# Optimization experiments

Measured on AMD Instinct MI355X. Metric: run time of the kernel, lower is better.

The kernel has to match this reference:

```python
import jax, jax.numpy as jnp
import numpy as np
from functools import partial

C_IN = 32
KT = 10  # 3*3 taps + bias


def avgpool(x, k):
    B, C, H, W = x.shape
    return x.reshape(B, C, H // k, k, W // k, k).mean(axis=(3, 5))


def conv3x3(x, w, b):
    out = jax.lax.conv_general_dilated(
        x, w, window_strides=(1, 1), padding=[(1, 1), (1, 1)],
        dimension_numbers=("NCHW", "OIHW", "NCHW"))
    return out + b[None, :, None, None]


def conv1x1(x, w, b):
    # w: [O, C, 1, 1]
    return jnp.einsum("bchw,oc->bohw", x, w[:, :, 0, 0]) + b[None, :, None, None]


def predictor(x, w1, b1, w2, b2):
    return x + conv3x3(jax.nn.leaky_relu(conv3x3(x, w1, b1), 0.01), w2, b2)


def flying_conv(x, weight, bias):
    # x: [B,C,H,W]; weight: [B,C,Hb,Wb,9]; bias: [B,C,Hb,Wb]; 8x8 blocks
    B, C, H, W = x.shape
    Hb, Wb = H // 8, W // 8
    xp = jnp.pad(x, ((0, 0), (0, 0), (1, 1), (1, 1)))
    out = jnp.broadcast_to(bias[:, :, :, None, :, None], (B, C, Hb, 8, Wb, 8))
    for k in range(9):
        di, dj = k // 3, k % 3
        xs = xp[:, :, di:di + H, dj:dj + W].reshape(B, C, Hb, 8, Wb, 8)
        out = out + xs * weight[:, :, :, None, :, None, k]
    return out.reshape(B, C, H, W)


def setup_inputs() -> dict:
    key = jax.random.key(0)
    ks = jax.random.split(key, 5)
    B, C, H, W = 4, C_IN, 512, 512
    x = jax.random.normal(ks[0], (B, C, H, W), dtype=jnp.float32)
    pa_w = jax.random.normal(ks[1], (4, 2, C, C, 3, 3), dtype=jnp.float32) * 0.05
    pa_b = jnp.zeros((4, 2, C), dtype=jnp.float32)
    exp_w = jax.random.normal(ks[2], (C * KT, C, 1, 1), dtype=jnp.float32) * 0.05
    exp_b = jnp.zeros((C * KT,), dtype=jnp.float32)
    pw_w = jax.random.normal(ks[3], (C, C, 1, 1), dtype=jnp.float32) * 0.1
    pw_b = jnp.zeros((C,), dtype=jnp.float32)
    return {"x": x, "pa_w": pa_w, "pa_b": pa_b, "exp_w": exp_w,
            "exp_b": exp_b, "pw_w": pw_w, "pw_b": pw_b}


def reference(x, pa_w, pa_b, exp_w, exp_b, pw_w, pw_b):
    B, C, H, W = x.shape
    feat = avgpool(x, 4)  # H/4
    for i in range(4):
        feat = predictor(feat, pa_w[i, 0], pa_b[i, 0], pa_w[i, 1], pa_b[i, 1])
        if i == 1:
            feat = avgpool(feat, 2)  # -> H/8
    wmap = conv1x1(feat, exp_w, exp_b)  # [B, C*10, Hb, Wb]
    Hb, Wb = H // 8, W // 8
    wmap = jnp.tanh(wmap.reshape(B, C, KT, Hb, Wb).transpose(0, 1, 3, 4, 2))
    weight, bias = wmap[..., :9], wmap[..., 9]
    out = flying_conv(x, weight, bias)
    return conv1x1(out, pw_w, pw_b)
```

## Files before the change

kernel.cpp:

```cpp
#include <hip/hip_runtime.h>


#define BATCH 4
#define NCH 32
#define CS128 17680
#define SP128 136
#define CS64 4752
#define SP64 72

__device__ __forceinline__ float fast_tanh(float s) {
  float e = __expf(2.f * s);
  return fmaf(-2.f, __builtin_amdgcn_rcpf(e + 1.f), 1.f);
}

__global__ void zero_kernel(float* __restrict__ p) {
  int i = blockIdx.x * 256 + threadIdx.x;
  *reinterpret_cast<float4*>(p + (size_t)i * 4) = make_float4(0.f, 0.f, 0.f, 0.f);
}

__global__ void prep_kernel(const float* __restrict__ pa_w, const float* __restrict__ exp_w,
                            const float* __restrict__ pw_w, float* __restrict__ wt,
                            float* __restrict__ ewt, float* __restrict__ pwt) {
  int i = blockIdx.x * 256 + threadIdx.x;
  if (i < 73728) {
    int tap = i % 9; int t = i / 9;
    int ci = t & 31; t >>= 5;
    int co = t & 31; int layer = t >> 5;
    wt[((layer * 32 + ci) * 9 + tap) * 32 + co] = pa_w[i];
  } else if (i < 83968) {
    int j = i - 73728; int ci = j & 31; int o = j >> 5;
    ewt[ci * 320 + o] = exp_w[j];
  } else if (i < 84992) {
    int j = i - 83968; int c = j & 31; int o = j >> 5;
    pwt[c * 32 + o] = pw_w[j];
  }
}

__global__ void avgpool4_kernel(const float* __restrict__ x, float* __restrict__ outp) {
  int idx = blockIdx.x * 256 + threadIdx.x;
  if (idx >= BATCH * NCH * 128 * 128) return;
  int ow = idx & 127; int t = idx >> 7; int oh = t & 127; int bc = t >> 7;
  const float* src = x + ((size_t)(bc * 512 + oh * 4)) * 512 + ow * 4;
  float s = 0.f;
#pragma unroll
  for (int r = 0; r < 4; r++) {
    float4 v = *reinterpret_cast<const float4*>(src + (size_t)r * 512);
    s += v.x + v.y + v.z + v.w;
  }
  outp[(size_t)bc * CS128 + (size_t)(oh + 1) * SP128 + ow + 4] = s * 0.0625f;
}

__global__ void avgpool2_kernel(const float* __restrict__ inp, float* __restrict__ outp) {
  int idx = blockIdx.x * 256 + threadIdx.x;
  if (idx >= BATCH * NCH * 64 * 64) return;
  int ow = idx & 63; int t = idx >> 6; int oh = t & 63; int bc = t >> 6;
  const float* sp = inp + (size_t)bc * CS128 + (size_t)(2 * oh + 1) * SP128 + 2 * ow + 4;
  float2 a = *reinterpret_cast<const float2*>(sp);
  float2 b = *reinterpret_cast<const float2*>(sp + SP128);
  outp[(size_t)bc * CS64 + (size_t)(oh + 1) * SP64 + ow + 4] = (a.x + a.y + b.x + b.y) * 0.25f;
}

template <int HS, int SP, int CS, int NCO, bool RELU, bool RES>
__global__ __launch_bounds__(256) void conv3x3d_kernel(
    const float* __restrict__ in, const float* __restrict__ wt,
    const float* __restrict__ bias, const float* __restrict__ res,
    float* __restrict__ out) {
  constexpr int TILES = HS / 16;
  constexpr int GROUPS = 32 / NCO;
  int blk = blockIdx.x;
  int g = blk % GROUPS; int rest = blk / GROUPS;
  int b = rest / (TILES * TILES); int t = rest % (TILES * TILES);
  int ty = t / TILES, tx = t % TILES;
  int og = g * NCO;
  int px = threadIdx.x & 15, py = threadIdx.x >> 4;
  int gy = ty * 16 + py, gx = tx * 16 + px;
  size_t pix = (size_t)(gy + 1) * SP + gx + 4;
  const float* inb = in + (size_t)b * 32 * CS + pix;

  float acc[NCO];
#pragma unroll
  for (int o = 0; o < NCO; o++) acc[o] = bias[og + o];

#pragma unroll 2
  for (int ci = 0; ci < 32; ci++) {
    const float* p = inb + (size_t)ci * CS;
    float v[9];
    v[0] = p[-SP - 1]; v[1] = p[-SP]; v[2] = p[-SP + 1];
    v[3] = p[-1];      v[4] = p[0];   v[5] = p[1];
    v[6] = p[SP - 1];  v[7] = p[SP];  v[8] = p[SP + 1];
    const float* wr = wt + ci * 288 + og;
#pragma unroll
    for (int tap = 0; tap < 9; tap++) {
      const float* wrow = wr + tap * 32;
#pragma unroll
      for (int o = 0; o < NCO; o++)
        acc[o] = fmaf(v[tap], wrow[o], acc[o]);
    }
  }

  float* ob = out + (size_t)b * 32 * CS + (size_t)og * CS + pix;
  const float* rb = RES ? (res + (size_t)b * 32 * CS + (size_t)og * CS + pix) : nullptr;
#pragma unroll
  for (int o = 0; o < NCO; o++) {
    float r2 = acc[o];
    if (RELU) r2 = r2 > 0.f ? r2 : 0.01f * r2;
    if (RES) r2 += rb[(size_t)o * CS];
    ob[(size_t)o * CS] = r2;
  }
}

__global__ __launch_bounds__(256) void expander_kernel(
    const float* __restrict__ feat, const float* __restrict__ ewt,
    const float* __restrict__ eb, float* __restrict__ wmap) {
  int idx = blockIdx.x * 256 + threadIdx.x;
  int wq = idx & 15; int t = idx >> 4;
  int o = t % 320; int rest = t / 320;
  int hb = rest & 63; int b = rest >> 6;
  const float* fp = feat + (size_t)b * 32 * CS64 + (size_t)(hb + 1) * SP64 + 4 + wq * 4;
  float s0 = eb[o];
  float s1 = s0, s2 = s0, s3 = s0;
#pragma unroll 8
  for (int ci = 0; ci < 32; ci++) {
    float4 f = *reinterpret_cast<const float4*>(fp + (size_t)ci * CS64);
    float wv = ewt[ci * 320 + o];
    s0 = fmaf(f.x, wv, s0); s1 = fmaf(f.y, wv, s1);
    s2 = fmaf(f.z, wv, s2); s3 = fmaf(f.w, wv, s3);
  }
  float4 r;
  r.x = fast_tanh(s0); r.y = fast_tanh(s1);
  r.z = fast_tanh(s2); r.w = fast_tanh(s3);
  *reinterpret_cast<float4*>(wmap + (size_t)((b * 64 + hb) * 320 + o) * 64 + wq * 4) = r;
}

__global__ __launch_bounds__(256) void fused_fly_pw_kernel(
    const float* __restrict__ x, const float* __restrict__ wmap,
    const float* __restrict__ pwt, const float* __restrict__ pw_b,
    float* __restrict__ out) {
  __shared__ float s_w[8][322];
  __shared__ float s_x[8][10][68];
  int blk = blockIdx.x;
  int wtile = blk & 7; int t = blk >> 3; int hb = t & 63; int b = t >> 6;
  int tid = threadIdx.x;

  const float* wsrc = wmap + (size_t)(b * 64 + hb) * 320 * 64 + wtile * 8;
#pragma unroll
  for (int j = 0; j < 10; j++) {
    int idx = j * 256 + tid;
    int tap = idx >> 3, wb8 = idx & 7;
    s_w[wb8][tap] = wsrc[(size_t)tap * 64 + wb8];
  }

  int p = tid & 31, row = tid >> 5;
  int h = hb * 8 + row;
  int w0 = wtile * 64 + 2 * p;
  int wbl = p >> 2;
  int h0 = hb * 8;
  int gc0 = wtile * 64 - 1;
  const float* xb = x + (size_t)b * 32 * 262144;

  int sch = tid >> 5, lane = tid & 31;
  int gxa = gc0 + lane, gxb = gc0 + lane + 32, gxc = gc0 + lane + 64;
  bool oka = (gxa >= 0);
  bool okc = (lane < 2) && (gxc < 512);

  float2 acc[32];
#pragma unroll
  for (int o = 0; o < 32; o++) {
    float bv = pw_b[o];
    acc[o].x = bv; acc[o].y = bv;
  }

  for (int g = 0; g < 4; g++) {
    __syncthreads();
    {
      const float* xc = xb + (size_t)(g * 8 + sch) * 262144;
      float* sxc = &s_x[sch][0][0];
#pragma unroll
      for (int rr = 0; rr < 10; rr++) {
        int gy = h0 - 1 + rr;
        bool oky = (gy >= 0) && (gy < 512);
        const float* rp = xc + (size_t)gy * 512;
        sxc[rr * 68 + lane]      = (oky && oka) ? rp[gxa] : 0.f;
        sxc[rr * 68 + lane + 32] = oky ? rp[gxb] : 0.f;
        if (lane < 2)
          sxc[rr * 68 + lane + 64] = (oky && okc) ? rp[gxc] : 0.f;
      }
    }
    __syncthreads();

#pragma unroll
    for (int c8 = 0; c8 < 8; c8++) {
      int c = g * 8 + c8;
      const float2* wr2 = reinterpret_cast<const float2*>(&s_w[wbl][c * 10]);
      float2 w01 = wr2[0], w23 = wr2[1], w45 = wr2[2], w67 = wr2[3], w89 = wr2[4];
      float wv[9];
      wv[0] = w01.x; wv[1] = w01.y; wv[2] = w23.x;
      wv[3] = w23.y; wv[4] = w45.x; wv[5] = w45.y;
      wv[6] = w67.x; wv[7] = w67.y; wv[8] = w89.x;
      float fly0 = w89.y, fly1 = w89.y;

#pragma unroll
      for (int di = 0; di < 3; di++) {
        const float2* rp = reinterpret_cast<const float2*>(&s_x[c8][row + di][2 * p]);
        float2 a = rp[0], bb = rp[1];
        float wa = wv[di * 3 + 0], wb_ = wv[di * 3 + 1], wc = wv[di * 3 + 2];
        fly0 = fmaf(a.x, wa, fly0); fly0 = fmaf(a.y, wb_, fly0); fly0 = fmaf(bb.x, wc, fly0);
        fly1 = fmaf(a.y, wa, fly1); fly1 = fmaf(bb.x, wb_, fly1); fly1 = fmaf(bb.y, wc, fly1);
      }
      const float* prow = pwt + c * 32;
#pragma unroll
      for (int o = 0; o < 32; o++) {
        float pw = prow[o];
        acc[o].x = fmaf(fly0, pw, acc[o].x);
        acc[o].y = fmaf(fly1, pw, acc[o].y);
      }
    }
  }
  float* ob = out + (size_t)b * 32 * 262144 + (size_t)h * 512 + w0;
#pragma unroll
  for (int o = 0; o < 32; o++)
    *reinterpret_cast<float2*>(ob + (size_t)o * 262144) = acc[o];
}

extern "C" void kernel_launch(void* const* d_in, const int* in_sizes, int n_in,
                              void* d_out, int out_size, void* d_ws, size_t ws_size,
                              hipStream_t stream) {
  const float* x     = (const float*)d_in[0];
  const float* pa_w  = (const float*)d_in[1];
  const float* pa_b  = (const float*)d_in[2];
  const float* exp_w = (const float*)d_in[3];
  const float* exp_b = (const float*)d_in[4];
  const float* pw_w  = (const float*)d_in[5];
  const float* pw_b  = (const float*)d_in[6];
  float* out = (float*)d_out;
  float* ws  = (float*)d_ws;

  float* feat0p = ws;
  float* tmpAp  = feat0p + 2263040;
  float* feat1p = tmpAp + 2263040;
  float* wmap   = feat1p + 608256;
  float* tmpBp  = wmap;
  float* wt     = wmap + 5242880;
  float* ewt    = wt + 73728;
  float* pwt    = ewt + 10240;

  hipLaunchKernelGGL(zero_kernel, dim3(5608), dim3(256), 0, stream, ws);
  hipLaunchKernelGGL(prep_kernel, dim3(332), dim3(256), 0, stream, pa_w, exp_w, pw_w, wt, ewt, pwt);
  hipLaunchKernelGGL(avgpool4_kernel, dim3(8192), dim3(256), 0, stream, x, feat0p);

  for (int i = 0; i < 2; i++) {
    const float* w1 = wt + (size_t)(i * 2 + 0) * 9216;
    const float* b1 = pa_b + (i * 2 + 0) * 32;
    const float* w2 = wt + (size_t)(i * 2 + 1) * 9216;
    const float* b2 = pa_b + (i * 2 + 1) * 32;
    hipLaunchKernelGGL((conv3x3d_kernel<128, SP128, CS128, 4, true, false>),
                       dim3(2048), dim3(256), 0, stream, feat0p, w1, b1, nullptr, tmpAp);
    hipLaunchKernelGGL((conv3x3d_kernel<128, SP128, CS128, 4, false, true>),
                       dim3(2048), dim3(256), 0, stream, tmpAp, w2, b2, feat0p, feat0p);
  }

  hipLaunchKernelGGL(avgpool2_kernel, dim3(2048), dim3(256), 0, stream, feat0p, feat1p);

  for (int i = 2; i < 4; i++) {
    const float* w1 = wt + (size_t)(i * 2 + 0) * 9216;
    const float* b1 = pa_b + (i * 2 + 0) * 32;
    const float* w2 = wt + (size_t)(i * 2 + 1) * 9216;
    const float* b2 = pa_b + (i * 2 + 1) * 32;
    hipLaunchKernelGGL((conv3x3d_kernel<64, SP64, CS64, 2, true, false>),
                       dim3(1024), dim3(256), 0, stream, feat1p, w1, b1, nullptr, tmpBp);
    hipLaunchKernelGGL((conv3x3d_kernel<64, SP64, CS64, 2, false, true>),
                       dim3(1024), dim3(256), 0, stream, tmpBp, w2, b2, feat1p, feat1p);
  }

  hipLaunchKernelGGL(expander_kernel, dim3(5120), dim3(256), 0, stream, feat1p, ewt, exp_b, wmap);

  hipLaunchKernelGGL(fused_fly_pw_kernel, dim3(2048), dim3(256), 0, stream,
                     x, wmap, pwt, pw_b, out);
}
```

Baseline: 389.1 us.

## Compute two rows per thread in 3x3 conv; read x directly in fly kernel

```diff
diff --git a/kernel.cpp b/kernel.cpp
--- a/kernel.cpp
+++ b/kernel.cpp
@@ -58,6 +58,60 @@
   float2 a = *reinterpret_cast<const float2*>(sp);
   float2 b = *reinterpret_cast<const float2*>(sp + SP128);
   outp[(size_t)bc * CS64 + (size_t)(oh + 1) * SP64 + ow + 4] = (a.x + a.y + b.x + b.y) * 0.25f;
+}
+
+template <int HS, int SP, int CS, int NCO, bool RELU, bool RES>
+__global__ __launch_bounds__(256) void conv3x3v_kernel(
+    const float* __restrict__ in, const float* __restrict__ wt,
+    const float* __restrict__ bias, const float* __restrict__ res,
+    float* __restrict__ out) {
+  constexpr int TX = HS / 16;
+  constexpr int TY = HS / 32;
+  constexpr int GROUPS = 32 / NCO;
+  int blk = blockIdx.x;
+  int g = blk % GROUPS; int rest = blk / GROUPS;
+  int b = rest / (TX * TY); int t = rest % (TX * TY);
+  int ty = t / TX, tx = t % TX;
+  int og = g * NCO;
+  int px = threadIdx.x & 15, py = threadIdx.x >> 4;
+  int gy = ty * 32 + py * 2, gx = tx * 16 + px;
+  size_t pix = (size_t)(gy + 1) * SP + gx + 4;
+  const float* inb = in + (size_t)b * 32 * CS + pix;
+
+  float acc0[NCO], acc1[NCO];
+#pragma unroll
+  for (int o = 0; o < NCO; o++) { acc0[o] = bias[og + o]; acc1[o] = acc0[o]; }
+
+#pragma unroll 2
+  for (int ci = 0; ci < 32; ci++) {
+    const float* p = inb + (size_t)ci * CS;
+    float v[12];
+    v[0] = p[-SP - 1];    v[1] = p[-SP];     v[2] = p[-SP + 1];
+    v[3] = p[-1];         v[4] = p[0];       v[5] = p[1];
+    v[6] = p[SP - 1];     v[7] = p[SP];      v[8] = p[SP + 1];
+    v[9] = p[2 * SP - 1]; v[10] = p[2 * SP]; v[11] = p[2 * SP + 1];
+    const float* wr = wt + ci * 288 + og;
+#pragma unroll
+    for (int tap = 0; tap < 9; tap++) {
+      const float* wrow = wr + tap * 32;
+#pragma unroll
+      for (int o = 0; o < NCO; o++) {
+        acc0[o] = fmaf(v[tap], wrow[o], acc0[o]);
+        acc1[o] = fmaf(v[tap + 3], wrow[o], acc1[o]);
+      }
+    }
+  }
+
+  float* ob = out + (size_t)b * 32 * CS + (size_t)og * CS + pix;
+  const float* rb = RES ? (res + (size_t)b * 32 * CS + (size_t)og * CS + pix) : nullptr;
+#pragma unroll
+  for (int o = 0; o < NCO; o++) {
+    float r0 = acc0[o], r1 = acc1[o];
+    if (RELU) { r0 = r0 > 0.f ? r0 : 0.01f * r0; r1 = r1 > 0.f ? r1 : 0.01f * r1; }
+    if (RES) { r0 += rb[(size_t)o * CS]; r1 += rb[(size_t)o * CS + SP]; }
+    ob[(size_t)o * CS] = r0;
+    ob[(size_t)o * CS + SP] = r1;
+  }
 }
 
 template <int HS, int SP, int CS, int NCO, bool RELU, bool RES>
@@ -137,7 +191,6 @@
     const float* __restrict__ pwt, const float* __restrict__ pw_b,
     float* __restrict__ out) {
   __shared__ float s_w[8][322];
-  __shared__ float s_x[8][10][68];
   int blk = blockIdx.x;
   int wtile = blk & 7; int t = blk >> 3; int hb = t & 63; int b = t >> 6;
   int tid = threadIdx.x;
@@ -149,19 +202,14 @@
     int tap = idx >> 3, wb8 = idx & 7;
     s_w[wb8][tap] = wsrc[(size_t)tap * 64 + wb8];
   }
+  __syncthreads();
 
   int p = tid & 31, row = tid >> 5;
   int h = hb * 8 + row;
   int w0 = wtile * 64 + 2 * p;
   int wbl = p >> 2;
-  int h0 = hb * 8;
-  int gc0 = wtile * 64 - 1;
   const float* xb = x + (size_t)b * 32 * 262144;
-
-  int sch = tid >> 5, lane = tid & 31;
-  int gxa = gc0 + lane, gxb = gc0 + lane + 32, gxc = gc0 + lane + 64;
-  bool oka = (gxa >= 0);
-  bool okc = (lane < 2) && (gxc < 512);
+  bool wl_ok = (w0 > 0), wr_ok = (w0 < 510);
 
   float2 acc[32];
 #pragma unroll
@@ -170,50 +218,34 @@
     acc[o].x = bv; acc[o].y = bv;
   }
 
-  for (int g = 0; g < 4; g++) {
-    __syncthreads();
-    {
-      const float* xc = xb + (size_t)(g * 8 + sch) * 262144;
-      float* sxc = &s_x[sch][0][0];
-#pragma unroll
-      for (int rr = 0; rr < 10; rr++) {
-        int gy = h0 - 1 + rr;
-        bool oky = (gy >= 0) && (gy < 512);
-        const float* rp = xc + (size_t)gy * 512;
-        sxc[rr * 68 + lane]      = (oky && oka) ? rp[gxa] : 0.f;
-        sxc[rr * 68 + lane + 32] = oky ? rp[gxb] : 0.f;
-        if (lane < 2)
-          sxc[rr * 68 + lane + 64] = (oky && okc) ? rp[gxc] : 0.f;
-      }
+  for (int c = 0; c < 32; c++) {
+    const float2* w2p = reinterpret_cast<const float2*>(&s_w[wbl][c * 10]);
+    float2 w01 = w2p[0], w23 = w2p[1], w45 = w2p[2], w67 = w2p[3], w89 = w2p[4];
+    float wv[9];
+    wv[0] = w01.x; wv[1] = w01.y; wv[2] = w23.x;
+    wv[3] = w23.y; wv[4] = w45.x; wv[5] = w45.y;
+    wv[6] = w67.x; wv[7] = w67.y; wv[8] = w89.x;
+    float fly0 = w89.y, fly1 = w89.y;
+
+    const float* xc = xb + (size_t)c * 262144;
+#pragma unroll
+    for (int di = 0; di < 3; di++) {
+      int hh = h + di - 1;
+      if (hh < 0 || hh >= 512) continue;
+      const float* rp = xc + (size_t)hh * 512 + w0;
+      float xl = wl_ok ? rp[-1] : 0.f;
+      float2 xm = *reinterpret_cast<const float2*>(rp);
+      float xr = wr_ok ? rp[2] : 0.f;
+      float wa = wv[di * 3 + 0], wb_ = wv[di * 3 + 1], wc = wv[di * 3 + 2];
+      fly0 = fmaf(xl,   wa, fly0); fly0 = fmaf(xm.x, wb_, fly0); fly0 = fmaf(xm.y, wc, fly0);
+      fly1 = fmaf(xm.x, wa, fly1); fly1 = fmaf(xm.y, wb_, fly1); fly1 = fmaf(xr,   wc, fly1);
     }
-    __syncthreads();
-
-#pragma unroll
-    for (int c8 = 0; c8 < 8; c8++) {
-      int c = g * 8 + c8;
-      const float2* wr2 = reinterpret_cast<const float2*>(&s_w[wbl][c * 10]);
-      float2 w01 = wr2[0], w23 = wr2[1], w45 = wr2[2], w67 = wr2[3], w89 = wr2[4];
-      float wv[9];
-      wv[0] = w01.x; wv[1] = w01.y; wv[2] = w23.x;
-      wv[3] = w23.y; wv[4] = w45.x; wv[5] = w45.y;
-      wv[6] = w67.x; wv[7] = w67.y; wv[8] = w89.x;
-      float fly0 = w89.y, fly1 = w89.y;
-
-#pragma unroll
-      for (int di = 0; di < 3; di++) {
-        const float2* rp = reinterpret_cast<const float2*>(&s_x[c8][row + di][2 * p]);
-        float2 a = rp[0], bb = rp[1];
-        float wa = wv[di * 3 + 0], wb_ = wv[di * 3 + 1], wc = wv[di * 3 + 2];
-        fly0 = fmaf(a.x, wa, fly0); fly0 = fmaf(a.y, wb_, fly0); fly0 = fmaf(bb.x, wc, fly0);
-        fly1 = fmaf(a.y, wa, fly1); fly1 = fmaf(bb.x, wb_, fly1); fly1 = fmaf(bb.y, wc, fly1);
-      }
-      const float* prow = pwt + c * 32;
-#pragma unroll
-      for (int o = 0; o < 32; o++) {
-        float pw = prow[o];
-        acc[o].x = fmaf(fly0, pw, acc[o].x);
-        acc[o].y = fmaf(fly1, pw, acc[o].y);
-      }
+    const float* prow = pwt + c * 32;
+#pragma unroll
+    for (int o = 0; o < 32; o++) {
+      float pw = prow[o];
+      acc[o].x = fmaf(fly0, pw, acc[o].x);
+      acc[o].y = fmaf(fly1, pw, acc[o].y);
     }
   }
   float* ob = out + (size_t)b * 32 * 262144 + (size_t)h * 512 + w0;
@@ -253,10 +285,10 @@
     const float* b1 = pa_b + (i * 2 + 0) * 32;
     const float* w2 = wt + (size_t)(i * 2 + 1) * 9216;
     const float* b2 = pa_b + (i * 2 + 1) * 32;
-    hipLaunchKernelGGL((conv3x3d_kernel<128, SP128, CS128, 4, true, false>),
-                       dim3(2048), dim3(256), 0, stream, feat0p, w1, b1, nullptr, tmpAp);
-    hipLaunchKernelGGL((conv3x3d_kernel<128, SP128, CS128, 4, false, true>),
-                       dim3(2048), dim3(256), 0, stream, tmpAp, w2, b2, feat0p, feat0p);
+    hipLaunchKernelGGL((conv3x3v_kernel<128, SP128, CS128, 4, true, false>),
+                       dim3(1024), dim3(256), 0, stream, feat0p, w1, b1, nullptr, tmpAp);
+    hipLaunchKernelGGL((conv3x3v_kernel<128, SP128, CS128, 4, false, true>),
+                       dim3(1024), dim3(256), 0, stream, tmpAp, w2, b2, feat0p, feat0p);
   }
 
   hipLaunchKernelGGL(avgpool2_kernel, dim3(2048), dim3(256), 0, stream, feat0p, feat1p);
```

New measurement: 331.0 us, median of 2. 1.18x faster.
